# Performance work log

Measured on AMD Instinct MI355X. Metric: run time of the kernel, lower is better.

Reference implementation:

```python
import jax, jax.numpy as jnp
import numpy as np
from jax import lax

W = 50      # window size
EPS = 1e-5  # BatchNorm eps (torch default)


def setup_inputs() -> dict:
    key = jax.random.key(0)
    ks = jax.random.split(key, 40)
    def n(i, shape, s=0.1):
        return (jax.random.normal(ks[i], shape, dtype=jnp.float32) * s).astype(jnp.float32)
    inp = {}
    inp['x'] = jax.random.normal(ks[0], (16, 1, 2048), dtype=jnp.float32)
    # conv stack (eval-mode BatchNorm: running mean/var are params)
    inp['conv1_w'] = n(1, (64, 1, 9));  inp['conv1_b'] = n(2, (64,))
    inp['bn1_g'] = 1.0 + n(3, (64,));   inp['bn1_b'] = n(4, (64,))
    inp['bn1_m'] = n(5, (64,));         inp['bn1_v'] = 0.5 + jax.random.uniform(ks[6], (64,), dtype=jnp.float32)
    inp['conv2_w'] = n(7, (32, 64, 7)); inp['conv2_b'] = n(8, (32,))
    inp['bn2_g'] = 1.0 + n(9, (32,));   inp['bn2_b'] = n(10, (32,))
    inp['bn2_m'] = n(11, (32,));        inp['bn2_v'] = 0.5 + jax.random.uniform(ks[12], (32,), dtype=jnp.float32)
    inp['conv3_w'] = n(13, (16, 32, 5)); inp['conv3_b'] = n(14, (16,))
    inp['bn3_g'] = 1.0 + n(15, (16,));   inp['bn3_b'] = n(16, (16,))
    inp['bn3_m'] = n(17, (16,));         inp['bn3_v'] = 0.5 + jax.random.uniform(ks[18], (16,), dtype=jnp.float32)
    # 2-layer LSTM, hidden 64, input 16 (torch gate order i,f,g,o)
    H = 64
    inp['wih0'] = n(19, (4 * H, 16)); inp['whh0'] = n(20, (4 * H, H))
    inp['bih0'] = n(21, (4 * H,));    inp['bhh0'] = n(22, (4 * H,))
    inp['wih1'] = n(23, (4 * H, H));  inp['whh1'] = n(24, (4 * H, H))
    inp['bih1'] = n(25, (4 * H,));    inp['bhh1'] = n(26, (4 * H,))
    # classifier 64 -> 32 -> 2
    inp['fc1_w'] = n(27, (32, H)); inp['fc1_b'] = n(28, (32,))
    inp['fc2_w'] = n(29, (2, 32)); inp['fc2_b'] = n(30, (2,))
    return inp


def _conv1d(x, w, b, pad):
    # x: [N, Cin, L], w: [Cout, Cin, K]
    y = lax.conv_general_dilated(x, w, (1,), [(pad, pad)],
                                 dimension_numbers=('NCH', 'OIH', 'NCH'))
    return y + b[:, None]


def _bn(x, g, b, m, v):
    # eval-mode BatchNorm1d over channel dim of [N, C, L]
    return (x - m[:, None]) * (g / jnp.sqrt(v + EPS))[:, None] + b[:, None]


def _lstm_layer(x, wih, whh, bih, bhh):
    # x: [B, T, D] -> [B, T, H]; torch gate order (i, f, g, o)
    B, T, D = x.shape
    H = whh.shape[1]
    xs = jnp.transpose(x, (1, 0, 2))                     # [T, B, D]
    pre = xs @ wih.T + (bih + bhh)                       # [T, B, 4H] input projection, hoisted
    def step(carry, p):
        h, c = carry
        g = p + h @ whh.T
        i, f, gg, o = jnp.split(g, 4, axis=-1)
        c = jax.nn.sigmoid(f) * c + jax.nn.sigmoid(i) * jnp.tanh(gg)
        h = jax.nn.sigmoid(o) * jnp.tanh(c)
        return (h, c), h
    h0 = jnp.zeros((B, H), x.dtype)
    _, hs = lax.scan(step, (h0, h0), pre)
    return jnp.transpose(hs, (1, 0, 2))


def reference(x, conv1_w, conv1_b, bn1_g, bn1_b, bn1_m, bn1_v,
              conv2_w, conv2_b, bn2_g, bn2_b, bn2_m, bn2_v,
              conv3_w, conv3_b, bn3_g, bn3_b, bn3_m, bn3_v,
              wih0, whh0, bih0, bhh0, wih1, whh1, bih1, bhh1,
              fc1_w, fc1_b, fc2_w, fc2_b):
    B, C, T = x.shape
    # sliding windows with left zero-pad of W-1 -> [B, T, C, W]
    xp = jnp.pad(x, ((0, 0), (0, 0), (W - 1, 0)))
    idx = jnp.arange(T)[:, None] + jnp.arange(W)[None, :]  # [T, W]
    win = xp[:, :, idx]                                    # [B, C, T, W]
    win = jnp.transpose(win, (0, 2, 1, 3)).reshape(B * T, C, W)
    # conv -> BN(eval) -> ReLU stack (dropout is identity in eval)
    h = jax.nn.relu(_bn(_conv1d(win, conv1_w, conv1_b, 4), bn1_g, bn1_b, bn1_m, bn1_v))
    h = jax.nn.relu(_bn(_conv1d(h, conv2_w, conv2_b, 3), bn2_g, bn2_b, bn2_m, bn2_v))
    h = jax.nn.relu(_bn(_conv1d(h, conv3_w, conv3_b, 2), bn3_g, bn3_b, bn3_m, bn3_v))
    feats = h.mean(axis=-1).reshape(B, T, -1)              # AdaptiveAvgPool1d(1) -> [B, T, 16]
    # 2-layer LSTM
    h1 = _lstm_layer(feats, wih0, whh0, bih0, bhh0)
    h2 = _lstm_layer(h1, wih1, whh1, bih1, bhh1)           # [B, T, 64]
    # classifier
    z = jax.nn.relu(h2 @ fc1_w.T + fc1_b)
    logits = z @ fc2_w.T + fc2_b                           # [B, T, 2]
    return logits
```

## Files before the change

### kernel.cpp

```cpp
#include <hip/hip_runtime.h>

#define EPSV 1e-5f
#define SCOPE_AGENT __HIP_MEMORY_SCOPE_AGENT

__device__ __forceinline__ float fast_rcp(float x) { return __builtin_amdgcn_rcpf(x); }
__device__ __forceinline__ float tanhfast(float x) {
    float e = __expf(2.0f * x);
    return 1.0f - 2.0f * fast_rcp(e + 1.0f);
}
__device__ __forceinline__ float dot4(const float4 w, const float4 v, float a) {
    a = fmaf(w.x, v.x, a);
    a = fmaf(w.y, v.y, a);
    a = fmaf(w.z, v.z, a);
    a = fmaf(w.w, v.w, a);
    return a;
}
#define DPPF(v, ctrl) __int_as_float(__builtin_amdgcn_mov_dpp(__float_as_int(v), (ctrl), 0xF, 0xF, false))

typedef unsigned long long ull;

struct RecS {
    float hbuf[2][80];
    float ring[16][64];
    float xst[16][80];
};
struct EdgeS {
    float A1[64 * 40];
    float A2[32 * 32];
    float xeL[24], xeR[24];
    float s1[64], t1[64], s2[32], t2[32], s3[16], t3[16];
    float psumE[288];
    float pi[512];
};

__global__ void pack_kernel(const float* __restrict__ w2, const float* __restrict__ w3,
                            float* __restrict__ w2t2, float4* __restrict__ w3p4,
                            float* __restrict__ w3p1, int* __restrict__ sync_ints) {
    int j = blockIdx.x * 256 + threadIdx.x;
    if (j < 16384) {
        int i = j >> 8;
        int o = (j >> 3) & 31;
        int k = j & 7;
        w2t2[j] = (k < 7) ? w2[o * 448 + i * 7 + k] : 0.0f;
    } else if (j < 16896) {
        int e = j - 16384;
        int i = e >> 4, o = e & 15;
        int base = o * 160 + i * 5;
        w3p4[e] = make_float4(w3[base], w3[base + 1], w3[base + 2], w3[base + 3]);
        w3p1[e] = w3[base + 4];
    } else if (j < 16896 + 4096) {
        sync_ints[j - 16896] = 0;
    }
}

__global__ __launch_bounds__(256) void conv1f_kernel(
    const float* __restrict__ x, const float* __restrict__ w1,
    const float* __restrict__ b1, const float* __restrict__ g1,
    const float* __restrict__ be1, const float* __restrict__ m1,
    const float* __restrict__ vv1, float* __restrict__ a1f)
{
    __shared__ float xs[72];
    const int tid = threadIdx.x;
    const int T = blockIdx.x * 64;
    const int b = blockIdx.y;
    if (tid < 72) {
        int gi = T - 49 + tid;
        xs[tid] = (gi >= 0 && gi < 2048) ? x[b * 2048 + gi] : 0.0f;
    }
    const int i = tid & 63, q = tid >> 6;
    float wv[9];
    #pragma unroll
    for (int k = 0; k < 9; ++k) wv[k] = w1[i * 9 + k];
    float sc = g1[i] * rsqrtf(vv1[i] + EPSV);
    float tc = (b1[i] - m1[i]) * sc + be1[i];
    __syncthreads();
    #pragma unroll
    for (int r = 0; r < 16; ++r) {
        int v1 = T + q * 16 + r;
        if (v1 < 2089) {
            float acc = 0.0f;
            #pragma unroll
            for (int k = 0; k < 9; ++k) acc = fmaf(wv[k], xs[q * 16 + r + k], acc);
            a1f[((long)b * 2089 + v1) * 64 + i] = fmaxf(acc * sc + tc, 0.0f);
        }
    }
}

__global__ __launch_bounds__(256) void conv2f_kernel(
    const float* __restrict__ a1f, const float* __restrict__ w2t2,
    const float* __restrict__ b2, const float* __restrict__ g2,
    const float* __restrict__ be2, const float* __restrict__ m2,
    const float* __restrict__ vv2, float* __restrict__ a2f)
{
    __shared__ __align__(16) float As[64 * 104];
    const int tid = threadIdx.x;
    const int T = blockIdx.x * 64;
    const int b = blockIdx.y;
    for (int idx = tid; idx < 1120; idx += 256) {
        int j = idx >> 4, i4 = (idx & 15) * 4;
        int v1 = T + j; if (v1 > 2088) v1 = 2088;
        float4 f = *(const float4*)&a1f[((long)b * 2089 + v1) * 64 + i4];
        int sj = j + ((j >> 3) << 2);
        As[(i4 + 0) * 104 + sj] = f.x;
        As[(i4 + 1) * 104 + sj] = f.y;
        As[(i4 + 2) * 104 + sj] = f.z;
        As[(i4 + 3) * 104 + sj] = f.w;
    }
    const int o = tid >> 3, pg = tid & 7;
    float sc = g2[o] * rsqrtf(vv2[o] + EPSV);
    float tc = (b2[o] - m2[o]) * sc + be2[o];
    __syncthreads();
    float acc[8];
    #pragma unroll
    for (int q = 0; q < 8; ++q) acc[q] = 0.0f;
    for (int i = 0; i < 64; ++i) {
        const float* rowp = &As[i * 104 + 12 * pg];
        float4 A0 = *(const float4*)&rowp[0];
        float4 A1 = *(const float4*)&rowp[4];
        float4 A2 = *(const float4*)&rowp[12];
        float2 A3 = *(const float2*)&rowp[16];
        const float4* wp = (const float4*)&w2t2[(i * 32 + o) * 8];
        float4 Wa = wp[0], Wb = wp[1];
        float av[14] = {A0.x, A0.y, A0.z, A0.w, A1.x, A1.y, A1.z, A1.w,
                        A2.x, A2.y, A2.z, A2.w, A3.x, A3.y};
        float wk[7] = {Wa.x, Wa.y, Wa.z, Wa.w, Wb.x, Wb.y, Wb.z};
        #pragma unroll
        for (int k = 0; k < 7; ++k) {
            #pragma unroll
            for (int q = 0; q < 8; ++q) acc[q] = fmaf(wk[k], av[q + k], acc[q]);
        }
    }
    #pragma unroll
    for (int q = 0; q < 8; ++q) {
        int v2 = T + pg * 8 + q;
        if (v2 < 2083)
            a2f[((long)b * 2083 + v2) * 32 + o] = fmaxf(acc[q] * sc + tc, 0.0f);
    }
}

__global__ __launch_bounds__(256) void conv3f_kernel(
    const float* __restrict__ a2f,
    const float4* __restrict__ w3p4, const float* __restrict__ w3p1,
    const float* __restrict__ b3, const float* __restrict__ g3,
    const float* __restrict__ be3, const float* __restrict__ m3,
    const float* __restrict__ vv3, float* __restrict__ a3f)
{
    __shared__ __align__(16) float A2s[32 * 200];
    const int tid = threadIdx.x;
    const int T = blockIdx.x * 128;
    const int b = blockIdx.y;
    for (int idx = tid; idx < 1056; idx += 256) {
        int j = idx >> 3, i4 = (idx & 7) * 4;
        int v2 = T + j; if (v2 > 2082) v2 = 2082;
        float4 f = *(const float4*)&a2f[((long)b * 2083 + v2) * 32 + i4];
        int sj = j + ((j >> 3) << 2);
        A2s[(i4 + 0) * 200 + sj] = f.x;
        A2s[(i4 + 1) * 200 + sj] = f.y;
        A2s[(i4 + 2) * 200 + sj] = f.z;
        A2s[(i4 + 3) * 200 + sj] = f.w;
    }
    const int o = tid & 15, pg = tid >> 4;
    float sc = g3[o] * rsqrtf(vv3[o] + EPSV);
    float tc = (b3[o] - m3[o]) * sc + be3[o];
    __syncthreads();
    float acc[8];
    #pragma unroll
    for (int q = 0; q < 8; ++q) acc[q] = 0.0f;
    for (int i = 0; i < 32; ++i) {
        const float* rowp = &A2s[i * 200 + 12 * pg];
        float4 R0 = *(const float4*)&rowp[0];
        float4 R1 = *(const float4*)&rowp[4];
        float4 R2 = *(const float4*)&rowp[12];
        float av[12] = {R0.x, R0.y, R0.z, R0.w, R1.x, R1.y, R1.z, R1.w,
                        R2.x, R2.y, R2.z, R2.w};
        float4 wa = w3p4[i * 16 + o];
        float w4 = w3p1[i * 16 + o];
        #pragma unroll
        for (int q = 0; q < 8; ++q) {
            acc[q] = fmaf(wa.x, av[q], acc[q]);
            acc[q] = fmaf(wa.y, av[q + 1], acc[q]);
            acc[q] = fmaf(wa.z, av[q + 2], acc[q]);
            acc[q] = fmaf(wa.w, av[q + 3], acc[q]);
            acc[q] = fmaf(w4,   av[q + 4], acc[q]);
        }
    }
    #pragma unroll
    for (int q = 0; q < 8; ++q) {
        int v3 = T + pg * 8 + q;
        if (v3 < 2079)
            a3f[((long)b * 2080 + v3) * 16 + o] = fmaxf(acc[q] * sc + tc, 0.0f);
        else if (v3 < 2080)
            a3f[((long)b * 2080 + v3) * 16 + o] = 0.0f;
    }
}

__device__ __forceinline__ void rec0_body(char* smemraw, int b,
    const float* __restrict__ feats,
    const float* __restrict__ wih, const float* __restrict__ whh,
    const float* __restrict__ bih, const float* __restrict__ bhh,
    float* __restrict__ hout, int* __restrict__ cnt0, int* __restrict__ flag1)
{
    RecS* s = (RecS*)smemraw;
    const int tid = threadIdx.x;
    const int j = tid >> 2, kq = tid & 3;

    const float4* pa = (const float4*)(whh + (0 * 64 + j) * 64 + kq * 16);
    const float4* pb = (const float4*)(whh + (1 * 64 + j) * 64 + kq * 16);
    const float4* pc_ = (const float4*)(whh + (2 * 64 + j) * 64 + kq * 16);
    const float4* pd = (const float4*)(whh + (3 * 64 + j) * 64 + kq * 16);
    float4 A0 = pa[0], A1 = pa[1], A2 = pa[2], A3 = pa[3];
    float4 B0 = pb[0], B1 = pb[1], B2 = pb[2], B3 = pb[3];
    float4 C0 = pc_[0], C1 = pc_[1], C2 = pc_[2], C3 = pc_[3];
    float4 D0 = pd[0], D1 = pd[1], D2 = pd[2], D3 = pd[3];
    float4 xw0 = *(const float4*)(wih + (0 * 64 + j) * 16 + kq * 4);
    float4 xw1 = *(const float4*)(wih + (1 * 64 + j) * 16 + kq * 4);
    float4 xw2 = *(const float4*)(wih + (2 * 64 + j) * 16 + kq * 4);
    float4 xw3 = *(const float4*)(wih + (3 * 64 + j) * 16 + kq * 4);
    const float bb0 = bih[j] + bhh[j];
    const float bb1 = bih[64 + j] + bhh[64 + j];
    const float bb2 = bih[128 + j] + bhh[128 + j];
    const float bb3 = bih[192 + j] + bhh[192 + j];

    if (tid < 64) s->hbuf[1][(tid >> 4) * 20 + (tid & 15)] = 0.0f;
    float cst = 0.0f;
    const float* fbase = feats + (long)b * 32768;
    __syncthreads();

#define STEP0(k) { \
        const float4* hp_ = (const float4*)&s->hbuf[((k) + 1) & 1][kq * 20]; \
        float4 h0_ = hp_[0], h1_ = hp_[1], h2_ = hp_[2], h3_ = hp_[3]; \
        float4 xv_ = *(const float4*)&s->xst[(k)][kq * 4]; \
        float p0 = dot4(A3, h3_, dot4(A2, h2_, dot4(A1, h1_, dot4(A0, h0_, dot4(xw0, xv_, 0.f))))); \
        float p1 = dot4(B3, h3_, dot4(B2, h2_, dot4(B1, h1_, dot4(B0, h0_, dot4(xw1, xv_, 0.f))))); \
        float p2 = dot4(C3, h3_, dot4(C2, h2_, dot4(C1, h1_, dot4(C0, h0_, dot4(xw2, xv_, 0.f))))); \
        float p3 = dot4(D3, h3_, dot4(D2, h2_, dot4(D1, h1_, dot4(D0, h0_, dot4(xw3, xv_, 0.f))))); \
        p0 += DPPF(p0, 0xB1); p1 += DPPF(p1, 0xB1); p2 += DPPF(p2, 0xB1); p3 += DPPF(p3, 0xB1); \
        p0 += DPPF(p0, 0x4E); p1 += DPPF(p1, 0x4E); p2 += DPPF(p2, 0x4E); p3 += DPPF(p3, 0x4E); \
        float gi = 1.0f - fast_rcp(__expf(p0 + bb0) + 1.0f); \
        float gf = 1.0f - fast_rcp(__expf(p1 + bb1) + 1.0f); \
        float gg = 1.0f - 2.0f * fast_rcp(__expf(2.0f * (p2 + bb2)) + 1.0f); \
        float go = 1.0f - fast_rcp(__expf(p3 + bb3) + 1.0f); \
        cst = fmaf(gf, cst, gi * gg); \
        float h_ = go * tanhfast(cst); \
        if (kq == 0) { s->hbuf[(k) & 1][(j >> 4) * 20 + (j & 15)] = h_; s->ring[(k)][j] = h_; } \
        __syncthreads(); \
    }

    for (int c = 0; c < 128; ++c) {
        if (tid == 0) {
            while (__hip_atomic_load(&cnt0[b * 128 + c], __ATOMIC_RELAXED, SCOPE_AGENT) < 16)
                __builtin_amdgcn_s_sleep(2);
        }
        __syncthreads();
        s->xst[tid >> 4][tid & 15] =
            __hip_atomic_load(fbase + c * 256 + tid, __ATOMIC_RELAXED, SCOPE_AGENT);
        __syncthreads();
        STEP0(0)  STEP0(1)  STEP0(2)  STEP0(3)
        STEP0(4)  STEP0(5)  STEP0(6)  STEP0(7)
        STEP0(8)  STEP0(9)  STEP0(10) STEP0(11)
        STEP0(12) STEP0(13) STEP0(14) STEP0(15)
        {
            ull* dst = (ull*)(hout + ((long)b * 2048 + c * 16) * 64);
            ull v0 = ((const ull*)s->ring)[tid];
            ull v1 = ((const ull*)s->ring)[tid + 256];
            __hip_atomic_store(dst + tid, v0, __ATOMIC_RELAXED, SCOPE_AGENT);
            __hip_atomic_store(dst + tid + 256, v1, __ATOMIC_RELAXED, SCOPE_AGENT);
            __syncthreads();
            if (tid == 0)
                __hip_atomic_store(&flag1[b * 128 + c], 1, __ATOMIC_RELAXED, SCOPE_AGENT);
        }
    }
#undef STEP0
}

__device__ __forceinline__ void rec1_body(char* smemraw, int b,
    const float* __restrict__ h1o,
    const float* __restrict__ wih, const float* __restrict__ whh,
    const float* __restrict__ bih, const float* __restrict__ bhh,
    float* __restrict__ hout, int* __restrict__ flag1)
{
    RecS* s = (RecS*)smemraw;
    const int tid = threadIdx.x;
    const int j = tid >> 2, kq = tid & 3;

    const float4* pa = (const float4*)(whh + (0 * 64 + j) * 64 + kq * 16);
    const float4* pb = (const float4*)(whh + (1 * 64 + j) * 64 + kq * 16);
    const float4* pc_ = (const float4*)(whh + (2 * 64 + j) * 64 + kq * 16);
    const float4* pd = (const float4*)(whh + (3 * 64 + j) * 64 + kq * 16);
    float4 A0 = pa[0], A1 = pa[1], A2 = pa[2], A3 = pa[3];
    float4 B0 = pb[0], B1 = pb[1], B2 = pb[2], B3 = pb[3];
    float4 C0 = pc_[0], C1 = pc_[1], C2 = pc_[2], C3 = pc_[3];
    float4 D0 = pd[0], D1 = pd[1], D2 = pd[2], D3 = pd[3];
    const float4* qa = (const float4*)(wih + (0 * 64 + j) * 64 + kq * 16);
    const float4* qb = (const float4*)(wih + (1 * 64 + j) * 64 + kq * 16);
    const float4* qc = (const float4*)(wih + (2 * 64 + j) * 64 + kq * 16);
    const float4* qd = (const float4*)(wih + (3 * 64 + j) * 64 + kq * 16);
    float4 XA0 = qa[0], XA1 = qa[1], XA2 = qa[2], XA3 = qa[3];
    float4 XB0 = qb[0], XB1 = qb[1], XB2 = qb[2], XB3 = qb[3];
    float4 XC0 = qc[0], XC1 = qc[1], XC2 = qc[2], XC3 = qc[3];
    float4 XD0 = qd[0], XD1 = qd[1], XD2 = qd[2], XD3 = qd[3];
    const float bb0 = bih[j] + bhh[j];
    const float bb1 = bih[64 + j] + bhh[64 + j];
    const float bb2 = bih[128 + j] + bhh[128 + j];
    const float bb3 = bih[192 + j] + bhh[192 + j];

    if (tid < 64) s->hbuf[1][(tid >> 4) * 20 + (tid & 15)] = 0.0f;
    float cst = 0.0f;
    __syncthreads();

#define STEP1(k) { \
        const float4* hp_ = (const float4*)&s->hbuf[((k) + 1) & 1][kq * 20]; \
        float4 h0_ = hp_[0], h1_ = hp_[1], h2_ = hp_[2], h3_ = hp_[3]; \
        const float4* xp_ = (const float4*)&s->xst[(k)][kq * 20]; \
        float4 x0_ = xp_[0], x1_ = xp_[1], x2_ = xp_[2], x3_ = xp_[3]; \
        float p0 = dot4(A3, h3_, dot4(A2, h2_, dot4(A1, h1_, dot4(A0, h0_, \
                   dot4(XA3, x3_, dot4(XA2, x2_, dot4(XA1, x1_, dot4(XA0, x0_, 0.f)))))))); \
        float p1 = dot4(B3, h3_, dot4(B2, h2_, dot4(B1, h1_, dot4(B0, h0_, \
                   dot4(XB3, x3_, dot4(XB2, x2_, dot4(XB1, x1_, dot4(XB0, x0_, 0.f)))))))); \
        float p2 = dot4(C3, h3_, dot4(C2, h2_, dot4(C1, h1_, dot4(C0, h0_, \
                   dot4(XC3, x3_, dot4(XC2, x2_, dot4(XC1, x1_, dot4(XC0, x0_, 0.f)))))))); \
        float p3 = dot4(D3, h3_, dot4(D2, h2_, dot4(D1, h1_, dot4(D0, h0_, \
                   dot4(XD3, x3_, dot4(XD2, x2_, dot4(XD1, x1_, dot4(XD0, x0_, 0.f)))))))); \
        p0 += DPPF(p0, 0xB1); p1 += DPPF(p1, 0xB1); p2 += DPPF(p2, 0xB1); p3 += DPPF(p3, 0xB1); \
        p0 += DPPF(p0, 0x4E); p1 += DPPF(p1, 0x4E); p2 += DPPF(p2, 0x4E); p3 += DPPF(p3, 0x4E); \
        float gi = 1.0f - fast_rcp(__expf(p0 + bb0) + 1.0f); \
        float gf = 1.0f - fast_rcp(__expf(p1 + bb1) + 1.0f); \
        float gg = 1.0f - 2.0f * fast_rcp(__expf(2.0f * (p2 + bb2)) + 1.0f); \
        float go = 1.0f - fast_rcp(__expf(p3 + bb3) + 1.0f); \
        cst = fmaf(gf, cst, gi * gg); \
        float h_ = go * tanhfast(cst); \
        if (kq == 0) { s->hbuf[(k) & 1][(j >> 4) * 20 + (j & 15)] = h_; s->ring[(k)][j] = h_; } \
        __syncthreads(); \
    }

    for (int c = 0; c < 128; ++c) {
        if (tid == 0) {
            while (__hip_atomic_load(&flag1[b * 128 + c], __ATOMIC_RELAXED, SCOPE_AGENT) < 1)
                __builtin_amdgcn_s_sleep(2);
        }
        __syncthreads();
        {
            const ull* src = (const ull*)(h1o + ((long)b * 2048 + c * 16) * 64);
            ull v0 = __hip_atomic_load(src + tid, __ATOMIC_RELAXED, SCOPE_AGENT);
            ull v1 = __hip_atomic_load(src + tid + 256, __ATOMIC_RELAXED, SCOPE_AGENT);
            int u0 = tid, u1 = tid + 256;
            int k0 = u0 >> 5, p0i = (u0 & 31) * 2;
            int k1 = u1 >> 5, p1i = (u1 & 31) * 2;
            *(ull*)&s->xst[k0][(p0i >> 4) * 20 + (p0i & 15)] = v0;
            *(ull*)&s->xst[k1][(p1i >> 4) * 20 + (p1i & 15)] = v1;
        }
        __syncthreads();
        STEP1(0)  STEP1(1)  STEP1(2)  STEP1(3)
        STEP1(4)  STEP1(5)  STEP1(6)  STEP1(7)
        STEP1(8)  STEP1(9)  STEP1(10) STEP1(11)
        STEP1(12) STEP1(13) STEP1(14) STEP1(15)
        {
            float4* dst = (float4*)(hout + ((long)b * 2048 + c * 16) * 64);
            dst[tid] = ((const float4*)s->ring)[tid];
        }
    }
#undef STEP1
}

__device__ __forceinline__ void edge_body(char* smemraw, int b, int t,
    const float* __restrict__ x,
    const float* __restrict__ w1,
    const float* __restrict__ b1, const float* __restrict__ g1,
    const float* __restrict__ be1, const float* __restrict__ m1, const float* __restrict__ vv1,
    const float* __restrict__ b2, const float* __restrict__ g2,
    const float* __restrict__ be2, const float* __restrict__ m2, const float* __restrict__ vv2,
    const float* __restrict__ b3, const float* __restrict__ g3,
    const float* __restrict__ be3, const float* __restrict__ m3, const float* __restrict__ vv3,
    const float* __restrict__ w2t2,
    const float4* __restrict__ w3p4, const float* __restrict__ w3p1,
    const float* __restrict__ a3f,
    float* __restrict__ feats, int* __restrict__ cnt0)
{
    EdgeS* s = (EdgeS*)smemraw;
    const int tid = threadIdx.x;

    if (tid < 128) {
        int dv = tid >> 2, o4 = (tid & 3) * 4;
        *(float4*)&s->pi[dv * 16 + o4] =
            *(const float4*)&a3f[((long)b * 2080 + t + dv) * 16 + o4];
    }
    if (tid < 64) {
        float sc = g1[tid] * rsqrtf(vv1[tid] + EPSV);
        s->s1[tid] = sc;
        s->t1[tid] = (b1[tid] - m1[tid]) * sc + be1[tid];
    } else if (tid < 96) {
        int o = tid - 64;
        float sc = g2[o] * rsqrtf(vv2[o] + EPSV);
        s->s2[o] = sc;
        s->t2[o] = (b2[o] - m2[o]) * sc + be2[o];
    } else if (tid < 112) {
        int o = tid - 96;
        float sc = g3[o] * rsqrtf(vv3[o] + EPSV);
        s->s3[o] = sc;
        s->t3[o] = (b3[o] - m3[o]) * sc + be3[o];
    } else if (tid < 136) {
        int j = tid - 112;
        float v = 0.0f;
        if (j >= 4 && j < 22) { int gi = t - 53 + j; if (gi >= 0) v = x[b * 2048 + gi]; }
        s->xeL[j] = v;
    } else if (tid < 160) {
        int j = tid - 136;
        float v = 0.0f;
        if (j <= 17) { int gi = t - 17 + j; if (gi >= 0) v = x[b * 2048 + gi]; }
        s->xeR[j] = v;
    }
    for (int idx = tid; idx < 384; idx += 256) {
        int o = idx / 6, z = idx - o * 6;
        s->A1[o * 40 + (z < 3 ? z : 31 + z)] = 0.0f;
    }
    if (tid < 128) {
        int o = tid >> 2, z = tid & 3;
        s->A2[o * 32 + (z < 2 ? z : 25 + z)] = 0.0f;
    }
    __syncthreads();

    {
        int o = tid >> 2, g = tid & 3;
        float wv[9];
        #pragma unroll
        for (int k = 0; k < 9; ++k) wv[k] = w1[o * 9 + k];
        float sc = s->s1[o], tc = s->t1[o];
        #pragma unroll
        for (int n = 0; n < 7; ++n) {
            int P = g * 7 + n;
            float acc = 0.0f;
            if (P < 14) {
                #pragma unroll
                for (int k = 0; k < 9; ++k) acc = fmaf(wv[k], s->xeL[P + k], acc);
                s->A1[o * 40 + 3 + P] = fmaxf(acc * sc + tc, 0.0f);
            } else {
                int pr = P - 14;
                #pragma unroll
                for (int k = 0; k < 9; ++k) acc = fmaf(wv[k], s->xeR[pr + k], acc);
                s->A1[o * 40 + 20 + pr] = fmaxf(acc * sc + tc, 0.0f);
            }
        }
    }
    __syncthreads();

    {
        int o = tid >> 3, g = tid & 7;
        int side = g >> 2, gg = g & 3;
        int be_ = gg * 3;
        int cnt = (gg == 3) ? 2 : 3;
        int beta0 = side ? 20 + be_ : be_;
        float acc0 = 0.f, acc1 = 0.f, acc2 = 0.f;
        for (int i = 0; i < 64; ++i) {
            const float* rp = &s->A1[i * 40 + beta0];
            float av[9];
            #pragma unroll
            for (int c = 0; c < 9; ++c) av[c] = rp[c];
            const float4* wp = (const float4*)&w2t2[(i * 32 + o) * 8];
            float4 Wa = wp[0], Wb = wp[1];
            float wk[7] = {Wa.x, Wa.y, Wa.z, Wa.w, Wb.x, Wb.y, Wb.z};
            #pragma unroll
            for (int k = 0; k < 7; ++k) {
                acc0 = fmaf(wk[k], av[k], acc0);
                acc1 = fmaf(wk[k], av[k + 1], acc1);
                acc2 = fmaf(wk[k], av[k + 2], acc2);
            }
        }
        float sc = s->s2[o], tc = s->t2[o];
        float r0 = fmaxf(acc0 * sc + tc, 0.0f);
        float r1 = fmaxf(acc1 * sc + tc, 0.0f);
        float r2 = fmaxf(acc2 * sc + tc, 0.0f);
        int base = o * 32 + (side ? 16 + be_ : 2 + be_);
        s->A2[base] = r0;
        s->A2[base + 1] = r1;
        if (cnt == 3) s->A2[base + 2] = r2;
    }
    __syncthreads();

    {
        int o = tid & 15, g = tid >> 4;
        float sc = s->s3[o], tc = s->t3[o];
        #pragma unroll
        for (int rep = 0; rep < 2; ++rep) {
            int P3 = (rep == 0) ? g : 16 + g;
            if (rep == 1 && g >= 2) break;
            int tb = (P3 >= 9) ? 16 + (P3 - 9) : P3;
            float acc = 0.0f;
            for (int i = 0; i < 32; ++i) {
                const float* rp = &s->A2[i * 32 + tb];
                float4 wa = w3p4[i * 16 + o];
                float w4 = w3p1[i * 16 + o];
                acc = fmaf(wa.x, rp[0], acc);
                acc = fmaf(wa.y, rp[1], acc);
                acc = fmaf(wa.z, rp[2], acc);
                acc = fmaf(wa.w, rp[3], acc);
                acc = fmaf(w4,   rp[4], acc);
            }
            s->psumE[P3 * 16 + o] = fmaxf(acc * sc + tc, 0.0f);
        }
    }
    __syncthreads();

    if (tid < 16) {
        float e = 0.0f;
        #pragma unroll
        for (int P3 = 0; P3 < 18; ++P3) e += s->psumE[P3 * 16 + tid];
        float ii = 0.0f;
        #pragma unroll
        for (int dv = 0; dv < 32; ++dv) ii += s->pi[dv * 16 + tid];
        __hip_atomic_store(&feats[((long)b * 2048 + t) * 16 + tid], (e + ii) * (1.0f / 50.0f),
                           __ATOMIC_RELAXED, SCOPE_AGENT);
    }
    __syncthreads();
    if (tid == 0)
        __hip_atomic_fetch_add(&cnt0[b * 128 + (t >> 4)], 1, __ATOMIC_RELAXED, SCOPE_AGENT);
}

__global__ __launch_bounds__(256, 2) void fused_kernel(
    const float* __restrict__ x,
    const float* __restrict__ w1, const float* __restrict__ b1,
    const float* __restrict__ g1, const float* __restrict__ be1,
    const float* __restrict__ m1, const float* __restrict__ vv1,
    const float* __restrict__ b2,
    const float* __restrict__ g2, const float* __restrict__ be2,
    const float* __restrict__ m2, const float* __restrict__ vv2,
    const float* __restrict__ b3,
    const float* __restrict__ g3, const float* __restrict__ be3,
    const float* __restrict__ m3, const float* __restrict__ vv3,
    const float* __restrict__ w2t2,
    const float4* __restrict__ w3p4, const float* __restrict__ w3p1,
    const float* __restrict__ a3f,
    const float* __restrict__ wih0, const float* __restrict__ whh0,
    const float* __restrict__ bih0, const float* __restrict__ bhh0,
    const float* __restrict__ wih1, const float* __restrict__ whh1,
    const float* __restrict__ bih1, const float* __restrict__ bhh1,
    float* __restrict__ feats, float* __restrict__ h1o, float* __restrict__ h2o,
    int* __restrict__ cnt0, int* __restrict__ flag1)
{
    __shared__ __align__(16) char smem[sizeof(EdgeS) > sizeof(RecS) ? sizeof(EdgeS) : sizeof(RecS)];

    if (blockIdx.x < 16) { rec0_body(smem, blockIdx.x, feats, wih0, whh0, bih0, bhh0, h1o, cnt0, flag1); return; }
    if (blockIdx.x < 32) { rec1_body(smem, blockIdx.x - 16, h1o, wih1, whh1, bih1, bhh1, h2o, flag1); return; }

    int w = blockIdx.x - 32;
    int b = w & 15;
    int t = w >> 4;
    edge_body(smem, b, t, x, w1, b1, g1, be1, m1, vv1, b2, g2, be2, m2, vv2,
              b3, g3, be3, m3, vv3, w2t2, w3p4, w3p1, a3f, feats, cnt0);
}

__global__ __launch_bounds__(256) void fc_kernel(
    const float* __restrict__ h2o,
    const float* __restrict__ fc1w, const float* __restrict__ fc1b,
    const float* __restrict__ fc2w, const float* __restrict__ fc2b,
    float* __restrict__ out)
{
    int r = blockIdx.x * 256 + threadIdx.x;
    float h[64];
    const float4* hp = (const float4*)(h2o + (long)r * 64);
    #pragma unroll
    for (int i = 0; i < 16; ++i) {
        float4 v = hp[i];
        h[4 * i] = v.x; h[4 * i + 1] = v.y; h[4 * i + 2] = v.z; h[4 * i + 3] = v.w;
    }
    float l0 = fc2b[0], l1 = fc2b[1];
    #pragma unroll 4
    for (int j = 0; j < 32; ++j) {
        float z = fc1b[j];
        #pragma unroll
        for (int k = 0; k < 64; ++k) z = fmaf(h[k], fc1w[j * 64 + k], z);
        z = fmaxf(z, 0.0f);
        l0 = fmaf(z, fc2w[j], l0);
        l1 = fmaf(z, fc2w[32 + j], l1);
    }
    out[r * 2] = l0;
    out[r * 2 + 1] = l1;
}

extern "C" void kernel_launch(void* const* d_in, const int* in_sizes, int n_in,
                              void* d_out, int out_size, void* d_ws, size_t ws_size,
                              hipStream_t stream) {
    const float* x    = (const float*)d_in[0];
    const float* w1   = (const float*)d_in[1];
    const float* b1   = (const float*)d_in[2];
    const float* g1   = (const float*)d_in[3];
    const float* be1  = (const float*)d_in[4];
    const float* m1   = (const float*)d_in[5];
    const float* v1   = (const float*)d_in[6];
    const float* w2   = (const float*)d_in[7];
    const float* b2   = (const float*)d_in[8];
    const float* g2   = (const float*)d_in[9];
    const float* be2  = (const float*)d_in[10];
    const float* m2   = (const float*)d_in[11];
    const float* v2   = (const float*)d_in[12];
    const float* w3   = (const float*)d_in[13];
    const float* b3   = (const float*)d_in[14];
    const float* g3   = (const float*)d_in[15];
    const float* be3  = (const float*)d_in[16];
    const float* m3   = (const float*)d_in[17];
    const float* v3   = (const float*)d_in[18];
    const float* wih0 = (const float*)d_in[19];
    const float* whh0 = (const float*)d_in[20];
    const float* bih0 = (const float*)d_in[21];
    const float* bhh0 = (const float*)d_in[22];
    const float* wih1 = (const float*)d_in[23];
    const float* whh1 = (const float*)d_in[24];
    const float* bih1 = (const float*)d_in[25];
    const float* bhh1 = (const float*)d_in[26];
    const float* fc1w = (const float*)d_in[27];
    const float* fc1b = (const float*)d_in[28];
    const float* fc2w = (const float*)d_in[29];
    const float* fc2b = (const float*)d_in[30];
    float* out = (float*)d_out;

    float* ws    = (float*)d_ws;
    float* feats = ws;
    float* h2o   = feats + 32768 * 16;
    float* w2t2  = h2o + 32768 * 64;
    float* w3p4f = w2t2 + 16384;
    float* w3p1  = w3p4f + 2048;
    float* h1o   = w3p1 + 512;
    float* a1f   = h1o + 32768 * 64;
    float* a2f   = a1f + 16 * 2089 * 64;
    float* a3f   = a2f + 16 * 2083 * 32;
    int*   cnt0  = (int*)(a3f + 16 * 2080 * 16);
    int*   flag1 = cnt0 + 2048;

    hipLaunchKernelGGL(pack_kernel, dim3(82), dim3(256), 0, stream,
                       w2, w3, w2t2, (float4*)w3p4f, w3p1, cnt0);
    hipLaunchKernelGGL(conv1f_kernel, dim3(33, 16), dim3(256), 0, stream,
                       x, w1, b1, g1, be1, m1, v1, a1f);
    hipLaunchKernelGGL(conv2f_kernel, dim3(33, 16), dim3(256), 0, stream,
                       a1f, w2t2, b2, g2, be2, m2, v2, a2f);
    hipLaunchKernelGGL(conv3f_kernel, dim3(17, 16), dim3(256), 0, stream,
                       a2f, (const float4*)w3p4f, w3p1, b3, g3, be3, m3, v3, a3f);
    hipLaunchKernelGGL(fused_kernel, dim3(32 + 32768), dim3(256), 0, stream,
                       x, w1, b1, g1, be1, m1, v1, b2, g2, be2, m2, v2,
                       b3, g3, be3, m3, v3, w2t2, (const float4*)w3p4f, w3p1, a3f,
                       wih0, whh0, bih0, bhh0, wih1, whh1, bih1, bhh1,
                       feats, h1o, h2o, cnt0, flag1);
    hipLaunchKernelGGL(fc_kernel, dim3(128), dim3(256), 0, stream,
                       h2o, fc1w, fc1b, fc2w, fc2b, out);
}
```

Baseline: 1.198 ms.

## Replace per-timestep edge blocks with batched GEMM edge stages and counters

Drops the one-block-per-timestep edge computation of the zero-padded window boundaries. It is replaced by register-tiled GEMMs over 64-timestep tiles using pre-packed banded conv2/conv3 weight matrices (left and right edges), followed by a small reduction stage that forms feats. The new stages chain through agent-scope atomic counters ahead of the LSTM consumers. The aim is to cut redundant per-window work and block count. In exchange it adds large intermediate buffers, an extra packing kernel and inter-block spin-waits whose ordering depends on block scheduling.

```diff
diff --git a/kernel.cpp b/kernel.cpp
--- a/kernel.cpp
+++ b/kernel.cpp
@@ -19,18 +19,29 @@
 
 typedef unsigned long long ull;
 
+__device__ __forceinline__ float aldf(const float* p) {
+    return __hip_atomic_load(p, __ATOMIC_RELAXED, SCOPE_AGENT);
+}
+__device__ __forceinline__ void astf(float* p, float v) {
+    __hip_atomic_store(p, v, __ATOMIC_RELAXED, SCOPE_AGENT);
+}
+__device__ __forceinline__ ull aldu(const ull* p) {
+    return __hip_atomic_load(p, __ATOMIC_RELAXED, SCOPE_AGENT);
+}
+__device__ __forceinline__ void astu(ull* p, ull v) {
+    __hip_atomic_store(p, v, __ATOMIC_RELAXED, SCOPE_AGENT);
+}
+
 struct RecS {
     float hbuf[2][80];
     float ring[16][64];
     float xst[16][80];
 };
-struct EdgeS {
-    float A1[64 * 40];
-    float A2[32 * 32];
-    float xeL[24], xeR[24];
-    float s1[64], t1[64], s2[32], t2[32], s3[16], t3[16];
-    float psumE[288];
-    float pi[512];
+struct GemS {
+    float Uc[32 * 72];
+    float xt[128];
+    float sc1[64], tc1[64];
+    float psum[64 * 16];
 };
 
 __global__ void pack_kernel(const float* __restrict__ w2, const float* __restrict__ w3,
@@ -48,8 +59,74 @@
         int base = o * 160 + i * 5;
         w3p4[e] = make_float4(w3[base], w3[base + 1], w3[base + 2], w3[base + 3]);
         w3p1[e] = w3[base + 4];
-    } else if (j < 16896 + 4096) {
+    } else if (j < 16896 + 5120) {
         sync_ints[j - 16896] = 0;
+    }
+}
+
+__global__ void pack_edgeW_kernel(const float* __restrict__ w2, const float* __restrict__ w3,
+                                  float* __restrict__ W2L, float* __restrict__ W2R,
+                                  float* __restrict__ W3L, float* __restrict__ W3R) {
+    int g = blockIdx.x * 256 + threadIdx.x;
+    if (g < 163840) {
+        int k = g >> 8, row = g & 255;
+        float v = 0.0f;
+        if (row < 224) {
+            int p = row >> 5, o = row & 31;
+            if (k < 256) {
+                int q = k >> 6, i = k & 63, j = q - p + 3;
+                if (j >= 0 && j <= 6) v = w2[o * 448 + i * 7 + j];
+            } else {
+                int d = (k - 256) >> 6, i = k & 63;
+                if (d <= p - 1) v = w2[o * 448 + i * 7 + (d + 7 - p)];
+            }
+        }
+        W2L[g] = v;
+    } else if (g < 327680) {
+        int e = g - 163840;
+        int k = e >> 8, row = e & 255;
+        float v = 0.0f;
+        if (row < 224) {
+            int pp = row >> 5, o = row & 31;
+            if (k < 384) {
+                int d = k >> 6, i = k & 63;
+                if (d >= pp && d - pp <= 6) v = w2[o * 448 + i * 7 + (d - pp)];
+            } else {
+                int qq = (k - 384) >> 6, i = k & 63;
+                if (qq <= pp) v = w2[o * 448 + i * 7 + (6 + qq - pp)];
+            }
+        }
+        W2R[e] = v;
+    } else if (g < 327680 + 114688) {
+        int e = g - 327680;
+        int k = e >> 8, row = e & 255;
+        float v = 0.0f;
+        if (row < 144) {
+            int p3 = row >> 4, o = row & 15;
+            if (k < 224) {
+                int pp_ = k >> 5, i = k & 31, m = pp_ - p3 + 2;
+                if (m >= 0 && m <= 4) v = w3[o * 160 + i * 5 + m];
+            } else {
+                int d = (k - 224) >> 5, i = k & 31, m = 9 + d - p3;
+                if (m >= 0 && m <= 4) v = w3[o * 160 + i * 5 + m];
+            }
+        }
+        W3L[e] = v;
+    } else if (g < 327680 + 114688 + 90112) {
+        int e = g - 327680 - 114688;
+        int k = e >> 8, row = e & 255;
+        float v = 0.0f;
+        if (row < 144) {
+            int pp3 = row >> 4, o = row & 15;
+            if (k < 128) {
+                int d = k >> 5, i = k & 31, m = d - pp3;
+                if (m >= 0 && m <= 4) v = w3[o * 160 + i * 5 + m];
+            } else {
+                int q = (k - 128) >> 5, i = k & 31, m = 4 + q - pp3;
+                if (m >= 0 && m <= 4) v = w3[o * 160 + i * 5 + m];
+            }
+        }
+        W3R[e] = v;
     }
 }
 
@@ -252,8 +329,7 @@
                 __builtin_amdgcn_s_sleep(2);
         }
         __syncthreads();
-        s->xst[tid >> 4][tid & 15] =
-            __hip_atomic_load(fbase + c * 256 + tid, __ATOMIC_RELAXED, SCOPE_AGENT);
+        s->xst[tid >> 4][tid & 15] = aldf(fbase + c * 256 + tid);
         __syncthreads();
         STEP0(0)  STEP0(1)  STEP0(2)  STEP0(3)
         STEP0(4)  STEP0(5)  STEP0(6)  STEP0(7)
@@ -263,8 +339,8 @@
             ull* dst = (ull*)(hout + ((long)b * 2048 + c * 16) * 64);
             ull v0 = ((const ull*)s->ring)[tid];
             ull v1 = ((const ull*)s->ring)[tid + 256];
-            __hip_atomic_store(dst + tid, v0, __ATOMIC_RELAXED, SCOPE_AGENT);
-            __hip_atomic_store(dst + tid + 256, v1, __ATOMIC_RELAXED, SCOPE_AGENT);
+            astu(dst + tid, v0);
+            astu(dst + tid + 256, v1);
             __syncthreads();
             if (tid == 0)
                 __hip_atomic_store(&flag1[b * 128 + c], 1, __ATOMIC_RELAXED, SCOPE_AGENT);
@@ -341,8 +417,8 @@
         __syncthreads();
         {
             const ull* src = (const ull*)(h1o + ((long)b * 2048 + c * 16) * 64);
-            ull v0 = __hip_atomic_load(src + tid, __ATOMIC_RELAXED, SCOPE_AGENT);
-            ull v1 = __hip_atomic_load(src + tid + 256, __ATOMIC_RELAXED, SCOPE_AGENT);
+            ull v0 = aldu(src + tid);
+            ull v1 = aldu(src + tid + 256);
             int u0 = tid, u1 = tid + 256;
             int k0 = u0 >> 5, p0i = (u0 & 31) * 2;
             int k1 = u1 >> 5, p1i = (u1 & 31) * 2;
@@ -362,190 +438,255 @@
 #undef STEP1
 }
 
-__device__ __forceinline__ void edge_body(char* smemraw, int b, int t,
-    const float* __restrict__ x,
-    const float* __restrict__ w1,
+__device__ void gemm_body(char* smemraw, int mode, int T, int b,
+    const float* __restrict__ x, const float* __restrict__ w1g,
     const float* __restrict__ b1, const float* __restrict__ g1,
     const float* __restrict__ be1, const float* __restrict__ m1, const float* __restrict__ vv1,
     const float* __restrict__ b2, const float* __restrict__ g2,
     const float* __restrict__ be2, const float* __restrict__ m2, const float* __restrict__ vv2,
     const float* __restrict__ b3, const float* __restrict__ g3,
     const float* __restrict__ be3, const float* __restrict__ m3, const float* __restrict__ vv3,
-    const float* __restrict__ w2t2,
-    const float4* __restrict__ w3p4, const float* __restrict__ w3p1,
+    const float* __restrict__ W2L, const float* __restrict__ W2R,
+    const float* __restrict__ W3L, const float* __restrict__ W3R,
+    const float* __restrict__ a1f, const float* __restrict__ a2f,
+    float* __restrict__ a2L, float* __restrict__ a2R,
+    float* __restrict__ edgeL, float* __restrict__ edgeR,
+    int* __restrict__ k2cnt, int* __restrict__ k3cnt)
+{
+    GemS* s = (GemS*)smemraw;
+    const int tid = threadIdx.x;
+    const int tg = tid >> 5, og = tid & 31;
+    const int t0 = T * 64;
+
+    if (mode <= 1) {
+        if (tid < 128) {
+            int gidx = t0 - 49 + tid;
+            s->xt[tid] = (tid < 116 && gidx >= 0 && gidx < 2048) ? x[b * 2048 + gidx] : 0.0f;
+        } else if (tid < 192) {
+            int i = tid - 128;
+            float sc = g1[i] * rsqrtf(vv1[i] + EPSV);
+            s->sc1[i] = sc;
+            s->tc1[i] = (b1[i] - m1[i]) * sc + be1[i];
+        }
+    } else {
+        if (mode == 2) {
+            if (tid == 0) {
+                while (__hip_atomic_load(&k2cnt[T * 16 + b], __ATOMIC_RELAXED, SCOPE_AGENT) < 2)
+                    __builtin_amdgcn_s_sleep(2);
+            }
+        } else {
+            if (tid == 0) {
+                while (__hip_atomic_load(&k2cnt[T * 16 + b], __ATOMIC_RELAXED, SCOPE_AGENT) < 2)
+                    __builtin_amdgcn_s_sleep(2);
+            }
+        }
+        for (int e = tid; e < 1024; e += 256) s->psum[e] = 0.0f;
+    }
+
+    float acc[8][8];
+    #pragma unroll
+    for (int a_ = 0; a_ < 8; ++a_)
+        #pragma unroll
+        for (int o_ = 0; o_ < 8; ++o_) acc[a_][o_] = 0.0f;
+
+    const int K = (mode <= 1) ? 640 : (mode == 2 ? 448 : 352);
+    const float* Wg = (mode == 0) ? W2L : (mode == 1) ? W2R : (mode == 2) ? W3L : W3R;
+    const int kst = tid >> 3, tb = (tid & 7) * 8;
+    __syncthreads();
+
+    for (int kc = 0; kc < K / 32; ++kc) {
+        #pragma unroll
+        for (int jj = 0; jj < 8; ++jj) {
+            int tl = tb + jj;
+            int col = kc * 32 + kst;
+            int t = t0 + tl;
+            float val;
+            if (mode == 0) {
+                if (col < 256) {
+                    int q = col >> 6, i = col & 63;
+                    float a = 0.0f;
+                    for (int kk = 4 - q; kk <= 8; ++kk)
+                        a = fmaf(w1g[i * 9 + kk], s->xt[tl + q + kk - 4], a);
+                    val = fmaxf(a * s->sc1[i] + s->tc1[i], 0.0f);
+                } else {
+                    int d = (col - 256) >> 6, i = col & 63;
+                    val = a1f[((long)b * 2089 + t + d) * 64 + i];
+                }
+            } else if (mode == 1) {
+                if (col < 384) {
+                    int d = col >> 6, i = col & 63;
+                    val = a1f[((long)b * 2089 + t + 36 + d) * 64 + i];
+                } else {
+                    int q = (col - 384) >> 6, i = col & 63;
+                    float a = 0.0f;
+                    for (int kk = 0; kk <= 7 - q; ++kk)
+                        a = fmaf(w1g[i * 9 + kk], s->xt[tl + 42 + q + kk], a);
+                    val = fmaxf(a * s->sc1[i] + s->tc1[i], 0.0f);
+                }
+            } else if (mode == 2) {
+                if (col < 224) val = aldf(a2L + ((long)b * 2048 + t) * 224 + col);
+                else {
+                    int d = (col - 224) >> 5;
+                    val = a2f[((long)b * 2083 + t + d) * 32 + (col & 31)];
+                }
+            } else {
+                if (col < 128) {
+                    int d = col >> 5;
+                    val = a2f[((long)b * 2083 + t + 32 + d) * 32 + (col & 31)];
+                } else val = aldf(a2R + ((long)b * 2048 + t) * 224 + (col - 128));
+            }
+            s->Uc[kst * 72 + tl] = val;
+        }
+        __syncthreads();
+        const float4* Wg4 = (const float4*)Wg;
+        #pragma unroll 4
+        for (int k = 0; k < 32; ++k) {
+            int ka = kc * 32 + k;
+            float4 w0 = Wg4[ka * 64 + og * 2];
+            float4 w1v = Wg4[ka * 64 + og * 2 + 1];
+            const float4* up = (const float4*)&s->Uc[k * 72 + tg * 8];
+            float4 u0 = up[0], u1 = up[1];
+            float ut[8] = {u0.x, u0.y, u0.z, u0.w, u1.x, u1.y, u1.z, u1.w};
+            float wo[8] = {w0.x, w0.y, w0.z, w0.w, w1v.x, w1v.y, w1v.z, w1v.w};
+            #pragma unroll
+            for (int a_ = 0; a_ < 8; ++a_)
+                #pragma unroll
+                for (int o_ = 0; o_ < 8; ++o_)
+                    acc[a_][o_] = fmaf(ut[a_], wo[o_], acc[a_][o_]);
+        }
+        __syncthreads();
+    }
+
+    if (mode <= 1) {
+        if (og <= 27) {
+            float s2v[8], t2v[8];
+            #pragma unroll
+            for (int oo = 0; oo < 8; ++oo) {
+                int o = (og * 8 + oo) & 31;
+                float sc = g2[o] * rsqrtf(vv2[o] + EPSV);
+                s2v[oo] = sc;
+                t2v[oo] = (b2[o] - m2[o]) * sc + be2[o];
+            }
+            float* dst = (mode == 0) ? a2L : a2R;
+            #pragma unroll
+            for (int tt = 0; tt < 8; ++tt) {
+                long base = ((long)b * 2048 + t0 + tg * 8 + tt) * 224 + og * 8;
+                #pragma unroll
+                for (int oo = 0; oo < 8; oo += 2) {
+                    float r0 = fmaxf(acc[tt][oo] * s2v[oo] + t2v[oo], 0.0f);
+                    float r1 = fmaxf(acc[tt][oo + 1] * s2v[oo + 1] + t2v[oo + 1], 0.0f);
+                    ull pv;
+                    ((float*)&pv)[0] = r0;
+                    ((float*)&pv)[1] = r1;
+                    astu((ull*)(dst + base + oo), pv);
+                }
+            }
+        }
+        __syncthreads();
+        if (tid == 0)
+            __hip_atomic_fetch_add(&k2cnt[T * 16 + b], 1, __ATOMIC_RELAXED, SCOPE_AGENT);
+    } else {
+        int p3 = og >> 1;
+        if (p3 <= 8) {
+            int obase = (og & 1) * 8;
+            float s3v[8], t3v[8];
+            #pragma unroll
+            for (int oo = 0; oo < 8; ++oo) {
+                int o = obase + oo;
+                float sc = g3[o] * rsqrtf(vv3[o] + EPSV);
+                s3v[oo] = sc;
+                t3v[oo] = (b3[o] - m3[o]) * sc + be3[o];
+            }
+            #pragma unroll
+            for (int tt = 0; tt < 8; ++tt) {
+                #pragma unroll
+                for (int oo = 0; oo < 8; ++oo) {
+                    float v = fmaxf(acc[tt][oo] * s3v[oo] + t3v[oo], 0.0f);
+                    atomicAdd(&s->psum[(tg * 8 + tt) * 16 + obase + oo], v);
+                }
+            }
+        }
+        __syncthreads();
+        {
+            float* dst = (mode == 2) ? edgeL : edgeR;
+            int tl = tid >> 2, o4 = (tid & 3) * 4;
+            long base = ((long)b * 2048 + t0 + tl) * 16 + o4;
+            const float* ps = &s->psum[tl * 16 + o4];
+            ull p0, p1;
+            ((float*)&p0)[0] = ps[0]; ((float*)&p0)[1] = ps[1];
+            ((float*)&p1)[0] = ps[2]; ((float*)&p1)[1] = ps[3];
+            astu((ull*)(dst + base), p0);
+            astu((ull*)(dst + base + 2), p1);
+        }
+        __syncthreads();
+        if (tid == 0)
+            __hip_atomic_fetch_add(&k3cnt[T * 16 + b], 1, __ATOMIC_RELAXED, SCOPE_AGENT);
+    }
+}
+
+__device__ void k4_body(int b, int c,
     const float* __restrict__ a3f,
-    float* __restrict__ feats, int* __restrict__ cnt0)
-{
-    EdgeS* s = (EdgeS*)smemraw;
+    const float* __restrict__ edgeL, const float* __restrict__ edgeR,
+    float* __restrict__ feats, int* __restrict__ cnt0, int* __restrict__ k3cnt)
+{
     const int tid = threadIdx.x;
-
-    if (tid < 128) {
-        int dv = tid >> 2, o4 = (tid & 3) * 4;
-        *(float4*)&s->pi[dv * 16 + o4] =
-            *(const float4*)&a3f[((long)b * 2080 + t + dv) * 16 + o4];
-    }
-    if (tid < 64) {
-        float sc = g1[tid] * rsqrtf(vv1[tid] + EPSV);
-        s->s1[tid] = sc;
-        s->t1[tid] = (b1[tid] - m1[tid]) * sc + be1[tid];
-    } else if (tid < 96) {
-        int o = tid - 64;
-        float sc = g2[o] * rsqrtf(vv2[o] + EPSV);
-        s->s2[o] = sc;
-        s->t2[o] = (b2[o] - m2[o]) * sc + be2[o];
-    } else if (tid < 112) {
-        int o = tid - 96;
-        float sc = g3[o] * rsqrtf(vv3[o] + EPSV);
-        s->s3[o] = sc;
-        s->t3[o] = (b3[o] - m3[o]) * sc + be3[o];
-    } else if (tid < 136) {
-        int j = tid - 112;
-        float v = 0.0f;
-        if (j >= 4 && j < 22) { int gi = t - 53 + j; if (gi >= 0) v = x[b * 2048 + gi]; }
-        s->xeL[j] = v;
-    } else if (tid < 160) {
-        int j = tid - 136;
-        float v = 0.0f;
-        if (j <= 17) { int gi = t - 17 + j; if (gi >= 0) v = x[b * 2048 + gi]; }
-        s->xeR[j] = v;
-    }
-    for (int idx = tid; idx < 384; idx += 256) {
-        int o = idx / 6, z = idx - o * 6;
-        s->A1[o * 40 + (z < 3 ? z : 31 + z)] = 0.0f;
-    }
-    if (tid < 128) {
-        int o = tid >> 2, z = tid & 3;
-        s->A2[o * 32 + (z < 2 ? z : 25 + z)] = 0.0f;
+    if (tid == 0) {
+        while (__hip_atomic_load(&k3cnt[(c >> 2) * 16 + b], __ATOMIC_RELAXED, SCOPE_AGENT) < 2)
+            __builtin_amdgcn_s_sleep(2);
     }
     __syncthreads();
-
-    {
-        int o = tid >> 2, g = tid & 3;
-        float wv[9];
-        #pragma unroll
-        for (int k = 0; k < 9; ++k) wv[k] = w1[o * 9 + k];
-        float sc = s->s1[o], tc = s->t1[o];
-        #pragma unroll
-        for (int n = 0; n < 7; ++n) {
-            int P = g * 7 + n;
-            float acc = 0.0f;
-            if (P < 14) {
-                #pragma unroll
-                for (int k = 0; k < 9; ++k) acc = fmaf(wv[k], s->xeL[P + k], acc);
-                s->A1[o * 40 + 3 + P] = fmaxf(acc * sc + tc, 0.0f);
-            } else {
-                int pr = P - 14;
-                #pragma unroll
-                for (int k = 0; k < 9; ++k) acc = fmaf(wv[k], s->xeR[pr + k], acc);
-                s->A1[o * 40 + 20 + pr] = fmaxf(acc * sc + tc, 0.0f);
-            }
-        }
-    }
-    __syncthreads();
-
-    {
-        int o = tid >> 3, g = tid & 7;
-        int side = g >> 2, gg = g & 3;
-        int be_ = gg * 3;
-        int cnt = (gg == 3) ? 2 : 3;
-        int beta0 = side ? 20 + be_ : be_;
-        float acc0 = 0.f, acc1 = 0.f, acc2 = 0.f;
-        for (int i = 0; i < 64; ++i) {
-            const float* rp = &s->A1[i * 40 + beta0];
-            float av[9];
-            #pragma unroll
-            for (int c = 0; c < 9; ++c) av[c] = rp[c];
-            const float4* wp = (const float4*)&w2t2[(i * 32 + o) * 8];
-            float4 Wa = wp[0], Wb = wp[1];
-            float wk[7] = {Wa.x, Wa.y, Wa.z, Wa.w, Wb.x, Wb.y, Wb.z};
-            #pragma unroll
-            for (int k = 0; k < 7; ++k) {
-                acc0 = fmaf(wk[k], av[k], acc0);
-                acc1 = fmaf(wk[k], av[k + 1], acc1);
-                acc2 = fmaf(wk[k], av[k + 2], acc2);
-            }
-        }
-        float sc = s->s2[o], tc = s->t2[o];
-        float r0 = fmaxf(acc0 * sc + tc, 0.0f);
-        float r1 = fmaxf(acc1 * sc + tc, 0.0f);
-        float r2 = fmaxf(acc2 * sc + tc, 0.0f);
-        int base = o * 32 + (side ? 16 + be_ : 2 + be_);
-        s->A2[base] = r0;
-        s->A2[base + 1] = r1;
-        if (cnt == 3) s->A2[base + 2] = r2;
-    }
-    __syncthreads();
-
-    {
-        int o = tid & 15, g = tid >> 4;
-        float sc = s->s3[o], tc = s->t3[o];
-        #pragma unroll
-        for (int rep = 0; rep < 2; ++rep) {
-            int P3 = (rep == 0) ? g : 16 + g;
-            if (rep == 1 && g >= 2) break;
-            int tb = (P3 >= 9) ? 16 + (P3 - 9) : P3;
-            float acc = 0.0f;
-            for (int i = 0; i < 32; ++i) {
-                const float* rp = &s->A2[i * 32 + tb];
-                float4 wa = w3p4[i * 16 + o];
-                float w4 = w3p1[i * 16 + o];
-                acc = fmaf(wa.x, rp[0], acc);
-                acc = fmaf(wa.y, rp[1], acc);
-                acc = fmaf(wa.z, rp[2], acc);
-                acc = fmaf(wa.w, rp[3], acc);
-                acc = fmaf(w4,   rp[4], acc);
-            }
-            s->psumE[P3 * 16 + o] = fmaxf(acc * sc + tc, 0.0f);
-        }
-    }
-    __syncthreads();
-
-    if (tid < 16) {
-        float e = 0.0f;
-        #pragma unroll
-        for (int P3 = 0; P3 < 18; ++P3) e += s->psumE[P3 * 16 + tid];
-        float ii = 0.0f;
-        #pragma unroll
-        for (int dv = 0; dv < 32; ++dv) ii += s->pi[dv * 16 + tid];
-        __hip_atomic_store(&feats[((long)b * 2048 + t) * 16 + tid], (e + ii) * (1.0f / 50.0f),
-                           __ATOMIC_RELAXED, SCOPE_AGENT);
-    }
+    int tt = tid >> 4, o = tid & 15;
+    int t = c * 16 + tt;
+    float sum = 0.0f;
+    #pragma unroll 8
+    for (int d = 0; d < 32; ++d) sum += a3f[((long)b * 2080 + t + d) * 16 + o];
+    sum += aldf(edgeL + ((long)b * 2048 + t) * 16 + o);
+    sum += aldf(edgeR + ((long)b * 2048 + t) * 16 + o);
+    astf(feats + ((long)b * 2048 + t) * 16 + o, sum * (1.0f / 50.0f));
     __syncthreads();
     if (tid == 0)
-        __hip_atomic_fetch_add(&cnt0[b * 128 + (t >> 4)], 1, __ATOMIC_RELAXED, SCOPE_AGENT);
+        __hip_atomic_fetch_add(&cnt0[b * 128 + c], 16, __ATOMIC_RELAXED, SCOPE_AGENT);
 }
 
 __global__ __launch_bounds__(256, 2) void fused_kernel(
-    const float* __restrict__ x,
-    const float* __restrict__ w1, const float* __restrict__ b1,
-    const float* __restrict__ g1, const float* __restrict__ be1,
-    const float* __restrict__ m1, const float* __restrict__ vv1,
-    const float* __restrict__ b2,
-    const float* __restrict__ g2, const float* __restrict__ be2,
-    const float* __restrict__ m2, const float* __restrict__ vv2,
-    const float* __restrict__ b3,
-    const float* __restrict__ g3, const float* __restrict__ be3,
-    const float* __restrict__ m3, const float* __restrict__ vv3,
-    const float* __restrict__ w2t2,
-    const float4* __restrict__ w3p4, const float* __restrict__ w3p1,
-    const float* __restrict__ a3f,
+    const float* __restrict__ x, const float* __restrict__ w1,
+    const float* __restrict__ b1, const float* __restrict__ g1,
+    const float* __restrict__ be1, const float* __restrict__ m1, const float* __restrict__ vv1,
+    const float* __restrict__ b2, const float* __restrict__ g2,
+    const float* __restrict__ be2, const float* __restrict__ m2, const float* __restrict__ vv2,
+    const float* __restrict__ b3, const float* __restrict__ g3,
+    const float* __restrict__ be3, const float* __restrict__ m3, const float* __restrict__ vv3,
+    const float* __restrict__ W2L, const float* __restrict__ W2R,
+    const float* __restrict__ W3L, const float* __restrict__ W3R,
+    const float* __restrict__ a1f, const float* __restrict__ a2f, const float* __restrict__ a3f,
+    float* __restrict__ a2L, float* __restrict__ a2R,
+    float* __restrict__ edgeL, float* __restrict__ edgeR,
     const float* __restrict__ wih0, const float* __restrict__ whh0,
     const float* __restrict__ bih0, const float* __restrict__ bhh0,
     const float* __restrict__ wih1, const float* __restrict__ whh1,
     const float* __restrict__ bih1, const float* __restrict__ bhh1,
     float* __restrict__ feats, float* __restrict__ h1o, float* __restrict__ h2o,
-    int* __restrict__ cnt0, int* __restrict__ flag1)
-{
-    __shared__ __align__(16) char smem[sizeof(EdgeS) > sizeof(RecS) ? sizeof(EdgeS) : sizeof(RecS)];
-
-    if (blockIdx.x < 16) { rec0_body(smem, blockIdx.x, feats, wih0, whh0, bih0, bhh0, h1o, cnt0, flag1); return; }
-    if (blockIdx.x < 32) { rec1_body(smem, blockIdx.x - 16, h1o, wih1, whh1, bih1, bhh1, h2o, flag1); return; }
-
-    int w = blockIdx.x - 32;
-    int b = w & 15;
-    int t = w >> 4;
-    edge_body(smem, b, t, x, w1, b1, g1, be1, m1, vv1, b2, g2, be2, m2, vv2,
-              b3, g3, be3, m3, vv3, w2t2, w3p4, w3p1, a3f, feats, cnt0);
+    int* __restrict__ cnt0, int* __restrict__ flag1,
+    int* __restrict__ k2cnt, int* __restrict__ k3cnt)
+{
+    __shared__ __align__(16) char smem[sizeof(GemS) > sizeof(RecS) ? sizeof(GemS) : sizeof(RecS)];
+
+    const int bid = blockIdx.x;
+    if (bid < 16) { rec0_body(smem, bid, feats, wih0, whh0, bih0, bhh0, h1o, cnt0, flag1); return; }
+    if (bid < 32) { rec1_body(smem, bid - 16, h1o, wih1, whh1, bih1, bhh1, h2o, flag1); return; }
+    int w = bid - 32;
+    int T = w >> 7;
+    int r = w & 127;
+    if (r < 64) {
+        int mode = r >> 4;
+        int b = r & 15;
+        gemm_body(smem, mode, T, b, x, w1, b1, g1, be1, m1, vv1,
+                  b2, g2, be2, m2, vv2, b3, g3, be3, m3, vv3,
+                  W2L, W2R, W3L, W3R, a1f, a2f, a2L, a2R, edgeL, edgeR, k2cnt, k3cnt);
+    } else {
+        int e = r - 64;
+        k4_body(e >> 2, T * 4 + (e & 3), a3f, edgeL, edgeR, feats, cnt0, k3cnt);
+    }
 }
 
 __global__ __launch_bounds__(256) void fc_kernel(
@@ -614,30 +755,45 @@
 
     float* ws    = (float*)d_ws;
     float* feats = ws;
-    float* h2o   = feats + 32768 * 16;
-    float* w2t2  = h2o + 32768 * 64;
+    float* h2o   = feats + 524288;
+    float* h1o   = h2o + 2097152;
+    float* w2t2  = h1o + 2097152;
     float* w3p4f = w2t2 + 16384;
     float* w3p1  = w3p4f + 2048;
-    float* h1o   = w3p1 + 512;
-    float* a1f   = h1o + 32768 * 64;
-    float* a2f   = a1f + 16 * 2089 * 64;
-    float* a3f   = a2f + 16 * 2083 * 32;
-    int*   cnt0  = (int*)(a3f + 16 * 2080 * 16);
-    int*   flag1 = cnt0 + 2048;
-
-    hipLaunchKernelGGL(pack_kernel, dim3(82), dim3(256), 0, stream,
-                       w2, w3, w2t2, (float4*)w3p4f, w3p1, cnt0);
+    float* a1f   = w3p1 + 512;
+    float* a2f   = a1f + 2139136;
+    float* a3f   = a2f + 1066496;
+    float* a2L   = a3f + 532480;
+    float* a2R   = a2L + 7340032;
+    float* edgeL = a2R + 7340032;
+    float* edgeR = edgeL + 524288;
+    float* W2L   = edgeR + 524288;
+    float* W2R   = W2L + 163840;
+    float* W3L   = W2R + 163840;
+    float* W3R   = W3L + 114688;
+    int*   sync_ = (int*)(W3R + 90112);
+    int*   cnt0  = sync_;
+    int*   flag1 = sync_ + 2048;
+    int*   k2cnt = sync_ + 4096;
+    int*   k3cnt = sync_ + 4608;
+
+    hipLaunchKernelGGL(pack_kernel, dim3(86), dim3(256), 0, stream,
+                       w2, w3, w2t2, (float4*)w3p4f, w3p1, sync_);
+    hipLaunchKernelGGL(pack_edgeW_kernel, dim3(2080), dim3(256), 0, stream,
+                       w2, w3, W2L, W2R, W3L, W3R);
     hipLaunchKernelGGL(conv1f_kernel, dim3(33, 16), dim3(256), 0, stream,
                        x, w1, b1, g1, be1, m1, v1, a1f);
     hipLaunchKernelGGL(conv2f_kernel, dim3(33, 16), dim3(256), 0, stream,
                        a1f, w2t2, b2, g2, be2, m2, v2, a2f);
     hipLaunchKernelGGL(conv3f_kernel, dim3(17, 16), dim3(256), 0, stream,
                        a2f, (const float4*)w3p4f, w3p1, b3, g3, be3, m3, v3, a3f);
-    hipLaunchKernelGGL(fused_kernel, dim3(32 + 32768), dim3(256), 0, stream,
-                       x, w1, b1, g1, be1, m1, v1, b2, g2, be2, m2, v2,
-                       b3, g3, be3, m3, v3, w2t2, (const float4*)w3p4f, w3p1, a3f,
+    hipLaunchKernelGGL(fused_kernel, dim3(32 + 32 * 128), dim3(256), 0, stream,
+                       x, w1, b1, g1, be1, m1, v1,
+                       b2, g2, be2, m2, v2, b3, g3, be3, m3, v3,
+                       W2L, W2R, W3L, W3R, a1f, a2f, a3f,
+                       a2L, a2R, edgeL, edgeR,
                        wih0, whh0, bih0, bhh0, wih1, whh1, bih1, bhh1,
-                       feats, h1o, h2o, cnt0, flag1);
+                       feats, h1o, h2o, cnt0, flag1, k2cnt, k3cnt);
     hipLaunchKernelGGL(fc_kernel, dim3(128), dim3(256), 0, stream,
                        h2o, fc1w, fc1b, fc2w, fc2b, out);
 }
```

Result: slower. 2.100 ms (+75.4%).
